# Kernel tuning notes

Hardware: AMD Instinct MI355X
Metric: run time of the kernel (lower is better)

## Reference

```python
import jax, jax.numpy as jnp
import numpy as np

H = 8          # n_heads
D_HEAD = 64    # head_dim; scores scaled by sqrt(D_HEAD)


def setup_inputs() -> dict:
    key = jax.random.key(0)
    ks = jax.random.split(key, 9)
    B, S, Dm = 8, 1024, 512
    return {
        "input_Q": jax.random.normal(ks[0], (B, S, Dm), jnp.float32),
        "input_K": jax.random.normal(ks[1], (B, S, Dm), jnp.float32),
        "input_V": jax.random.normal(ks[2], (B, S, Dm), jnp.float32),
        "attn_mask": jax.random.randint(ks[3], (B, S, S), 0, 2).astype(bool),
        "edge_encoding": jax.random.normal(ks[4], (B, S, S), jnp.float32),
        "W_Q": jax.random.normal(ks[5], (Dm, Dm), jnp.float32) / np.sqrt(Dm),
        "W_K": jax.random.normal(ks[6], (Dm, Dm), jnp.float32) / np.sqrt(Dm),
        "W_V": jax.random.normal(ks[7], (Dm, Dm), jnp.float32) / np.sqrt(Dm),
        "W_fc": jax.random.normal(ks[8], (Dm, Dm), jnp.float32) / np.sqrt(Dm),
    }


def reference(input_Q, input_K, input_V, attn_mask, edge_encoding, W_Q, W_K, W_V, W_fc):
    B, S, Dm = input_Q.shape
    # project and split heads: [B, H, S, d_head]
    def heads(x, W):
        return (x @ W).reshape(B, S, H, D_HEAD).transpose(0, 2, 1, 3)
    Q = heads(input_Q, W_Q)
    K = heads(input_K, W_K)
    V = heads(input_V, W_V)
    scores = jnp.einsum("bhqd,bhkd->bhqk", Q, K) / np.sqrt(D_HEAD)
    scores = scores + edge_encoding[:, None, :, :]
    scores = jnp.where(attn_mask[:, None, :, :], jnp.float32(-1e9), scores)
    attn = jax.nn.softmax(scores, axis=-1)
    context = jnp.einsum("bhqk,bhkd->bhqd", attn, V)
    context = context.transpose(0, 2, 1, 3).reshape(B, S, Dm)
    output = context @ W_fc
    scores_avg = scores.sum(axis=1) / H  # [B, S, S]
    return output, scores_avg
```

## Files before the change

### kernel.cpp

```cpp
#include <hip/hip_runtime.h>
#include <math.h>

#define B_ 8
#define S_ 1024
#define DM 512
#define H_ 8
#define DH 64

typedef _Float16 h4 __attribute__((ext_vector_type(4)));
typedef _Float16 h8 __attribute__((ext_vector_type(8)));
typedef float f4 __attribute__((ext_vector_type(4)));

#define MFMA16(a, b, c) __builtin_amdgcn_mfma_f32_16x16x32_f16(a, b, c, 0, 0, 0)

__global__ __launch_bounds__(256) void cast_x(
    const float* __restrict__ x0, const float* __restrict__ x1,
    const float* __restrict__ x2, _Float16* __restrict__ y0,
    _Float16* __restrict__ y1, _Float16* __restrict__ y2) {
  const float* x = (blockIdx.y == 0) ? x0 : (blockIdx.y == 1) ? x1 : x2;
  _Float16* y = (blockIdx.y == 0) ? y0 : (blockIdx.y == 1) ? y1 : y2;
  size_t i = (size_t)blockIdx.x * 1024 + (size_t)threadIdx.x * 4;
  float4 v = *(const float4*)(x + i);
  h4 hv = {(_Float16)v.x, (_Float16)v.y, (_Float16)v.z, (_Float16)v.w};
  *(h4*)(y + i) = hv;
}

__global__ __launch_bounds__(256) void cast_w(
    const float* __restrict__ w0, const float* __restrict__ w1,
    const float* __restrict__ w2, const float* __restrict__ w3,
    _Float16* __restrict__ t0, _Float16* __restrict__ t1,
    _Float16* __restrict__ t2, _Float16* __restrict__ t3) {
  const float* W;
  _Float16* T;
  switch (blockIdx.z) {
    case 0: W = w0; T = t0; break;
    case 1: W = w1; T = t1; break;
    case 2: W = w2; T = t2; break;
    default: W = w3; T = t3; break;
  }
  __shared__ _Float16 ts[64][72];
  const int t = threadIdx.x;
  const int r = t >> 2, c0 = (t & 3) * 16;
  const int n0 = blockIdx.x * 64, k0 = blockIdx.y * 64;
#pragma unroll
  for (int i = 0; i < 4; i++) {
    float4 v = *(const float4*)&W[(size_t)(k0 + r) * 512 + n0 + c0 + i * 4];
    h4 hv = {(_Float16)v.x, (_Float16)v.y, (_Float16)v.z, (_Float16)v.w};
    *(h4*)&ts[r][c0 + i * 4] = hv;
  }
  __syncthreads();
  alignas(16) _Float16 outv[16];
#pragma unroll
  for (int i = 0; i < 16; i++) outv[i] = ts[c0 + i][r];
  *(uint4*)&T[(size_t)(n0 + r) * 512 + k0 + c0] = *(uint4*)&outv[0];
  *(uint4*)&T[(size_t)(n0 + r) * 512 + k0 + c0 + 8] = *(uint4*)&outv[8];
}

__global__ __launch_bounds__(256) void gemm_qkv(
    const _Float16* __restrict__ Xq, const _Float16* __restrict__ Xk,
    const _Float16* __restrict__ Xv, const _Float16* __restrict__ Wt,
    _Float16* __restrict__ Qh, _Float16* __restrict__ Kh,
    _Float16* __restrict__ Vth) {
  const int z = blockIdx.z;
  const _Float16* A = (z == 0) ? Xq : (z == 1) ? Xk : Xv;
  const _Float16* Bt = Wt + (size_t)z * 512 * 512;
  __shared__ _Float16 As[128][72], Bs[128][72];
  const int t = threadIdx.x, lane = t & 63, w = t >> 6;
  const int quad = lane >> 4, l16 = lane & 15;
  const int row0 = blockIdx.y * 128, col0 = blockIdx.x * 128;
  const int wm = (w & 1) * 64, wn = (w >> 1) * 64;
  const int gr = t >> 3, gc = (t & 7) * 8;
  f4 acc[4][4] = {};
  uint4 pa[4], pb[4];
#pragma unroll
  for (int i = 0; i < 4; i++) {
    pa[i] = *(const uint4*)&A[(size_t)(row0 + gr + 32 * i) * DM + gc];
    pb[i] = *(const uint4*)&Bt[(size_t)(col0 + gr + 32 * i) * DM + gc];
  }
  for (int k0 = 0; k0 < DM; k0 += 64) {
    __syncthreads();
#pragma unroll
    for (int i = 0; i < 4; i++) {
      *(uint4*)&As[gr + 32 * i][gc] = pa[i];
      *(uint4*)&Bs[gr + 32 * i][gc] = pb[i];
    }
    __syncthreads();
    if (k0 + 64 < DM) {
#pragma unroll
      for (int i = 0; i < 4; i++) {
        pa[i] = *(const uint4*)&A[(size_t)(row0 + gr + 32 * i) * DM + k0 + 64 + gc];
        pb[i] = *(const uint4*)&Bt[(size_t)(col0 + gr + 32 * i) * DM + k0 + 64 + gc];
      }
    }
    h8 af[4][2], bf[4][2];
#pragma unroll
    for (int m = 0; m < 4; m++) {
      af[m][0] = *(h8*)&As[wm + m * 16 + l16][quad * 8];
      af[m][1] = *(h8*)&As[wm + m * 16 + l16][32 + quad * 8];
    }
#pragma unroll
    for (int n = 0; n < 4; n++) {
      bf[n][0] = *(h8*)&Bs[wn + n * 16 + l16][quad * 8];
      bf[n][1] = *(h8*)&Bs[wn + n * 16 + l16][32 + quad * 8];
    }
#pragma unroll
    for (int m = 0; m < 4; m++)
#pragma unroll
      for (int n = 0; n < 4; n++) {
        acc[m][n] = MFMA16(af[m][0], bf[n][0], acc[m][n]);
        acc[m][n] = MFMA16(af[m][1], bf[n][1], acc[m][n]);
      }
  }
  if (z < 2) {
    _Float16* C = (z == 0) ? Qh : Kh;
#pragma unroll
    for (int m = 0; m < 4; m++)
#pragma unroll
      for (int n = 0; n < 4; n++)
#pragma unroll
        for (int reg = 0; reg < 4; reg++) {
          size_t row = row0 + wm + m * 16 + quad * 4 + reg;
          size_t col = col0 + wn + n * 16 + l16;
          C[row * DM + col] = (_Float16)acc[m][n][reg];
        }
  } else {
#pragma unroll
    for (int m = 0; m < 4; m++)
#pragma unroll
      for (int n = 0; n < 4; n++) {
        int row = row0 + wm + m * 16 + quad * 4;
        int b = row >> 10, s = row & 1023;
        int col = col0 + wn + n * 16 + l16;
        int h = col >> 6, d = col & 63;
        h4 vv = {(_Float16)acc[m][n][0], (_Float16)acc[m][n][1],
                 (_Float16)acc[m][n][2], (_Float16)acc[m][n][3]};
        *(h4*)&Vth[((size_t)(b * 8 + h) * 64 + d) * S_ + s] = vv;
      }
  }
}

__global__ __launch_bounds__(256) void gemm_fc(
    const _Float16* __restrict__ A, const _Float16* __restrict__ Bt,
    float* __restrict__ C) {
  __shared__ _Float16 As[64][72], Bs[128][72];
  const int t = threadIdx.x, lane = t & 63, w = t >> 6;
  const int quad = lane >> 4, l16 = lane & 15;
  const int row0 = blockIdx.y * 64, col0 = blockIdx.x * 128;
  const int wm = (w & 1) * 32, wn = (w >> 1) * 64;
  const int gr = t >> 3, gc = (t & 7) * 8;
  f4 acc[2][4] = {};
  uint4 pa[2], pb[4];
#pragma unroll
  for (int i = 0; i < 2; i++)
    pa[i] = *(const uint4*)&A[(size_t)(row0 + gr + 32 * i) * DM + gc];
#pragma unroll
  for (int i = 0; i < 4; i++)
    pb[i] = *(const uint4*)&Bt[(size_t)(col0 + gr + 32 * i) * DM + gc];
  for (int k0 = 0; k0 < DM; k0 += 64) {
    __syncthreads();
#pragma unroll
    for (int i = 0; i < 2; i++) *(uint4*)&As[gr + 32 * i][gc] = pa[i];
#pragma unroll
    for (int i = 0; i < 4; i++) *(uint4*)&Bs[gr + 32 * i][gc] = pb[i];
    __syncthreads();
    if (k0 + 64 < DM) {
#pragma unroll
      for (int i = 0; i < 2; i++)
        pa[i] = *(const uint4*)&A[(size_t)(row0 + gr + 32 * i) * DM + k0 + 64 + gc];
#pragma unroll
      for (int i = 0; i < 4; i++)
        pb[i] = *(const uint4*)&Bt[(size_t)(col0 + gr + 32 * i) * DM + k0 + 64 + gc];
    }
    h8 af[2][2], bf[4][2];
#pragma unroll
    for (int m = 0; m < 2; m++) {
      af[m][0] = *(h8*)&As[wm + m * 16 + l16][quad * 8];
      af[m][1] = *(h8*)&As[wm + m * 16 + l16][32 + quad * 8];
    }
#pragma unroll
    for (int n = 0; n < 4; n++) {
      bf[n][0] = *(h8*)&Bs[wn + n * 16 + l16][quad * 8];
      bf[n][1] = *(h8*)&Bs[wn + n * 16 + l16][32 + quad * 8];
    }
#pragma unroll
    for (int m = 0; m < 2; m++)
#pragma unroll
      for (int n = 0; n < 4; n++) {
        acc[m][n] = MFMA16(af[m][0], bf[n][0], acc[m][n]);
        acc[m][n] = MFMA16(af[m][1], bf[n][1], acc[m][n]);
      }
  }
#pragma unroll
  for (int m = 0; m < 2; m++)
#pragma unroll
    for (int n = 0; n < 4; n++)
#pragma unroll
      for (int reg = 0; reg < 4; reg++) {
        size_t row = row0 + wm + m * 16 + quad * 4 + reg;
        size_t col = col0 + wn + n * 16 + l16;
        C[row * DM + col] = acc[m][n][reg];
      }
}

__global__ __launch_bounds__(256) void scores_mfma(
    const _Float16* __restrict__ Qh, const _Float16* __restrict__ Kh,
    const int* __restrict__ mask, const float* __restrict__ edge,
    float* __restrict__ out1, _Float16* __restrict__ Eh) {
  const int b = blockIdx.z;
  const int i0 = blockIdx.y * 128, j0 = blockIdx.x * 128;
  const _Float16* A = Qh + (size_t)b * S_ * DM;
  const _Float16* Bt = Kh + (size_t)b * S_ * DM;
  __shared__ _Float16 As[128][72], Bs[128][72];
  const int t = threadIdx.x, lane = t & 63, w = t >> 6;
  const int quad = lane >> 4, l16 = lane & 15;
  const int wm = (w & 1) * 64, wn = (w >> 1) * 64;
  const int gr = t >> 3, gc = (t & 7) * 8;
  f4 acc[4][4] = {};
  uint4 pa[4], pb[4];
#pragma unroll
  for (int i = 0; i < 4; i++) {
    pa[i] = *(const uint4*)&A[(size_t)(i0 + gr + 32 * i) * DM + gc];
    pb[i] = *(const uint4*)&Bt[(size_t)(j0 + gr + 32 * i) * DM + gc];
  }
  for (int k0 = 0; k0 < DM; k0 += 64) {
    __syncthreads();
#pragma unroll
    for (int i = 0; i < 4; i++) {
      *(uint4*)&As[gr + 32 * i][gc] = pa[i];
      *(uint4*)&Bs[gr + 32 * i][gc] = pb[i];
    }
    __syncthreads();
    if (k0 + 64 < DM) {
#pragma unroll
      for (int i = 0; i < 4; i++) {
        pa[i] = *(const uint4*)&A[(size_t)(i0 + gr + 32 * i) * DM + k0 + 64 + gc];
        pb[i] = *(const uint4*)&Bt[(size_t)(j0 + gr + 32 * i) * DM + k0 + 64 + gc];
      }
    }
    h8 af[4][2], bf[4][2];
#pragma unroll
    for (int m = 0; m < 4; m++) {
      af[m][0] = *(h8*)&As[wm + m * 16 + l16][quad * 8];
      af[m][1] = *(h8*)&As[wm + m * 16 + l16][32 + quad * 8];
    }
#pragma unroll
    for (int n = 0; n < 4; n++) {
      bf[n][0] = *(h8*)&Bs[wn + n * 16 + l16][quad * 8];
      bf[n][1] = *(h8*)&Bs[wn + n * 16 + l16][32 + quad * 8];
    }
#pragma unroll
    for (int m = 0; m < 4; m++)
#pragma unroll
      for (int n = 0; n < 4; n++) {
        acc[m][n] = MFMA16(af[m][0], bf[n][0], acc[m][n]);
        acc[m][n] = MFMA16(af[m][1], bf[n][1], acc[m][n]);
      }
  }
#pragma unroll
  for (int m = 0; m < 4; m++)
#pragma unroll
    for (int reg = 0; reg < 4; reg++) {
      size_t gi = i0 + wm + m * 16 + quad * 4 + reg;
      size_t rowb = ((size_t)b * S_ + gi) * S_;
#pragma unroll
      for (int n = 0; n < 4; n++) {
        size_t idx = rowb + j0 + wn + n * 16 + l16;
        int mk = mask[idx];
        float e = edge[idx];
        out1[idx] = mk ? -1e9f : (acc[m][n][reg] * (1.0f / 64.0f) + e);
        Eh[idx] = mk ? (_Float16)(-65504.0f) : (_Float16)e;
      }
    }
}

__global__ __launch_bounds__(256) void flash_mfma(
    const _Float16* __restrict__ Qh, const _Float16* __restrict__ Kh,
    const _Float16* __restrict__ Vth, const _Float16* __restrict__ Eh,
    _Float16* __restrict__ ctxh) {
  __shared__ _Float16 Ps[128][72], Ks[64][72], Vt[64][72];
  const int t = threadIdx.x, lane = t & 63, w = t >> 6;
  const int quad = lane >> 4, l16 = lane & 15;
  const int bh = blockIdx.y, b = bh >> 3, h = bh & 7;
  const int q0 = blockIdx.x * 128;
  const size_t bS = (size_t)b * S_;
  const int sr = t >> 3, sc = (t & 7) * 8;
  const int qw = w * 32;

#pragma unroll
  for (int i = 0; i < 4; i++)
    *(uint4*)&Ps[sr + 32 * i][sc] =
        *(const uint4*)&Qh[(bS + q0 + sr + 32 * i) * DM + h * DH + sc];
  __syncthreads();
  h8 aq[2][2];
#pragma unroll
  for (int m = 0; m < 2; m++)
#pragma unroll
    for (int k = 0; k < 2; k++)
      aq[m][k] = *(h8*)&Ps[qw + m * 16 + l16][k * 32 + quad * 8];

  uint4 kv[4];
  kv[0] = *(const uint4*)&Kh[(bS + sr) * DM + h * DH + sc];
  kv[1] = *(const uint4*)&Kh[(bS + sr + 32) * DM + h * DH + sc];
  kv[2] = *(const uint4*)&Vth[((size_t)bh * 64 + sr) * S_ + sc];
  kv[3] = *(const uint4*)&Vth[((size_t)bh * 64 + sr + 32) * S_ + sc];
  _Float16 evh[32];
#pragma unroll
  for (int m = 0; m < 2; m++)
#pragma unroll
    for (int n = 0; n < 4; n++)
#pragma unroll
      for (int reg = 0; reg < 4; reg++)
        evh[m * 16 + n * 4 + reg] =
            Eh[(bS + q0 + qw + m * 16 + quad * 4 + reg) * S_ + n * 16 + l16];

  f4 acco[2][4] = {};
  float m_run[2][4], l_run[2][4];
#pragma unroll
  for (int m = 0; m < 2; m++)
#pragma unroll
    for (int r = 0; r < 4; r++) {
      m_run[m][r] = -INFINITY;
      l_run[m][r] = 0.f;
    }

  for (int kb = 0; kb < S_; kb += 64) {
    __syncthreads();
    *(uint4*)&Ks[sr][sc] = kv[0];
    *(uint4*)&Ks[sr + 32][sc] = kv[1];
    *(uint4*)&Vt[sr][sc] = kv[2];
    *(uint4*)&Vt[sr + 32][sc] = kv[3];
    __syncthreads();
    const int kn = kb + 64;
    _Float16 evn[32];
    if (kn < S_) {
      kv[0] = *(const uint4*)&Kh[(bS + kn + sr) * DM + h * DH + sc];
      kv[1] = *(const uint4*)&Kh[(bS + kn + sr + 32) * DM + h * DH + sc];
      kv[2] = *(const uint4*)&Vth[((size_t)bh * 64 + sr) * S_ + kn + sc];
      kv[3] = *(const uint4*)&Vth[((size_t)bh * 64 + sr + 32) * S_ + kn + sc];
#pragma unroll
      for (int m = 0; m < 2; m++)
#pragma unroll
        for (int n = 0; n < 4; n++)
#pragma unroll
          for (int reg = 0; reg < 4; reg++)
            evn[m * 16 + n * 4 + reg] =
                Eh[(bS + q0 + qw + m * 16 + quad * 4 + reg) * S_ + kn +
                   n * 16 + l16];
    }
    f4 accs[2][4] = {};
#pragma unroll
    for (int n = 0; n < 4; n++) {
      h8 b0 = *(h8*)&Ks[n * 16 + l16][quad * 8];
      h8 b1 = *(h8*)&Ks[n * 16 + l16][32 + quad * 8];
#pragma unroll
      for (int m = 0; m < 2; m++) {
        accs[m][n] = MFMA16(aq[m][0], b0, accs[m][n]);
        accs[m][n] = MFMA16(aq[m][1], b1, accs[m][n]);
      }
    }
    float sv[2][4][4];
#pragma unroll
    for (int m = 0; m < 2; m++)
#pragma unroll
      for (int n = 0; n < 4; n++)
#pragma unroll
        for (int reg = 0; reg < 4; reg++)
          sv[m][n][reg] =
              accs[m][n][reg] * 0.125f + (float)evh[m * 16 + n * 4 + reg];
#pragma unroll
    for (int m = 0; m < 2; m++)
#pragma unroll
      for (int reg = 0; reg < 4; reg++) {
        float mx = fmaxf(fmaxf(sv[m][0][reg], sv[m][1][reg]),
                         fmaxf(sv[m][2][reg], sv[m][3][reg]));
#pragma unroll
        for (int off = 1; off < 16; off <<= 1)
          mx = fmaxf(mx, __shfl_xor(mx, off, 16));
        float mnew = fmaxf(m_run[m][reg], mx);
        float alpha = __expf(m_run[m][reg] - mnew);
        m_run[m][reg] = mnew;
        float psum = 0.f;
#pragma unroll
        for (int n = 0; n < 4; n++) {
          float p = __expf(sv[m][n][reg] - mnew);
          sv[m][n][reg] = p;
          psum += p;
        }
#pragma unroll
        for (int off = 1; off < 16; off <<= 1)
          psum += __shfl_xor(psum, off, 16);
        l_run[m][reg] = l_run[m][reg] * alpha + psum;
#pragma unroll
        for (int d = 0; d < 4; d++) acco[m][d][reg] *= alpha;
      }
#pragma unroll
    for (int m = 0; m < 2; m++)
#pragma unroll
      for (int n = 0; n < 4; n++)
#pragma unroll
        for (int reg = 0; reg < 4; reg++)
          Ps[qw + m * 16 + quad * 4 + reg][n * 16 + l16] =
              (_Float16)sv[m][n][reg];
    h8 ap[2][2];
#pragma unroll
    for (int m = 0; m < 2; m++)
#pragma unroll
      for (int k = 0; k < 2; k++)
        ap[m][k] = *(h8*)&Ps[qw + m * 16 + l16][k * 32 + quad * 8];
#pragma unroll
    for (int d = 0; d < 4; d++) {
      h8 bv0 = *(h8*)&Vt[d * 16 + l16][quad * 8];
      h8 bv1 = *(h8*)&Vt[d * 16 + l16][32 + quad * 8];
#pragma unroll
      for (int m = 0; m < 2; m++) {
        acco[m][d] = MFMA16(ap[m][0], bv0, acco[m][d]);
        acco[m][d] = MFMA16(ap[m][1], bv1, acco[m][d]);
      }
    }
    if (kn < S_) {
#pragma unroll
      for (int i = 0; i < 32; i++) evh[i] = evn[i];
    }
  }
#pragma unroll
  for (int m = 0; m < 2; m++)
#pragma unroll
    for (int d = 0; d < 4; d++)
#pragma unroll
      for (int reg = 0; reg < 4; reg++) {
        float o = acco[m][d][reg] / l_run[m][reg];
        ctxh[(bS + q0 + qw + m * 16 + quad * 4 + reg) * DM + h * DH + d * 16 +
             l16] = (_Float16)o;
      }
}

extern "C" void kernel_launch(void* const* d_in, const int* in_sizes, int n_in,
                              void* d_out, int out_size, void* d_ws,
                              size_t ws_size, hipStream_t stream) {
  const float* Xq = (const float*)d_in[0];
  const float* Xk = (const float*)d_in[1];
  const float* Xv = (const float*)d_in[2];
  const int* mask = (const int*)d_in[3];
  const float* edge = (const float*)d_in[4];
  const float* Wq = (const float*)d_in[5];
  const float* Wk = (const float*)d_in[6];
  const float* Wv = (const float*)d_in[7];
  const float* Wfc = (const float*)d_in[8];

  float* out0 = (float*)d_out;
  float* out1 = out0 + (size_t)B_ * S_ * DM;

  const size_t NE = (size_t)B_ * S_ * DM;
  char* ws = (char*)d_ws;
  _Float16* Qh = (_Float16*)ws;
  _Float16* Kh = Qh + NE;
  _Float16* Vth = Kh + NE;
  _Float16* Xhq = Vth + NE;
  _Float16* Xhk = Xhq + NE;
  _Float16* Xhv = Xhk + NE;
  _Float16* Wt = Xhv + NE;
  _Float16* Wtf = Wt + 3 * 512 * 512;
  _Float16* Eh = Wt + 4 * 512 * 512;
  _Float16* ctxh = Xhq;

  dim3 blk(256);
  cast_x<<<dim3(4096, 3), blk, 0, stream>>>(Xq, Xk, Xv, Xhq, Xhk, Xhv);
  cast_w<<<dim3(8, 8, 4), blk, 0, stream>>>(Wq, Wk, Wv, Wfc, Wt,
                                            Wt + 512 * 512, Wt + 2 * 512 * 512,
                                            Wtf);
  gemm_qkv<<<dim3(4, 64, 3), blk, 0, stream>>>(Xhq, Xhk, Xhv, Wt, Qh, Kh, Vth);
  scores_mfma<<<dim3(8, 8, 8), blk, 0, stream>>>(Qh, Kh, mask, edge, out1, Eh);
  flash_mfma<<<dim3(8, 64), blk, 0, stream>>>(Qh, Kh, Vth, Eh, ctxh);
  gemm_fc<<<dim3(4, 128), blk, 0, stream>>>(ctxh, Wtf, out0);
}
```

Baseline: 402.6 us.

## Tile edge-bias buffer per key block and remap block order for L2 locality

The fp16 edge/mask bias buffer is now written by the scores kernel in a tiled layout: per batch, per 64-key tile, per query row, with each lane's four columns stored contiguously. The flash kernel can then load them as h4 vectors instead of 32 scattered scalar fp16 loads per step. Block-index swizzles are also added to gemm_qkv, gemm_fc, scores and flash so that blocks scheduled together share operand tiles (heads of the same batch, neighbouring rows) in L2. The scores kernel's scattered fp16 writes become less coalesced, which is a possible cost.

Result: faster. 389.9 us (-3.2%).

```diff
diff --git a/kernel.cpp b/kernel.cpp
--- a/kernel.cpp
+++ b/kernel.cpp
@@ -62,12 +62,16 @@
     _Float16* __restrict__ Qh, _Float16* __restrict__ Kh,
     _Float16* __restrict__ Vth) {
   const int z = blockIdx.z;
+  const int id = blockIdx.x + 4 * blockIdx.y;
+  const int c = id & 7, r = id >> 3;
+  const int by = c + 8 * (r & 7);
+  const int bx = r >> 3;
   const _Float16* A = (z == 0) ? Xq : (z == 1) ? Xk : Xv;
   const _Float16* Bt = Wt + (size_t)z * 512 * 512;
   __shared__ _Float16 As[128][72], Bs[128][72];
   const int t = threadIdx.x, lane = t & 63, w = t >> 6;
   const int quad = lane >> 4, l16 = lane & 15;
-  const int row0 = blockIdx.y * 128, col0 = blockIdx.x * 128;
+  const int row0 = by * 128, col0 = bx * 128;
   const int wm = (w & 1) * 64, wn = (w >> 1) * 64;
   const int gr = t >> 3, gc = (t & 7) * 8;
   f4 acc[4][4] = {};
@@ -142,10 +146,14 @@
 __global__ __launch_bounds__(256) void gemm_fc(
     const _Float16* __restrict__ A, const _Float16* __restrict__ Bt,
     float* __restrict__ C) {
+  const int id = blockIdx.x + 4 * blockIdx.y;
+  const int c = id & 7, r = id >> 3;
+  const int by = c + 8 * (r & 15);
+  const int bx = r >> 4;
   __shared__ _Float16 As[64][72], Bs[128][72];
   const int t = threadIdx.x, lane = t & 63, w = t >> 6;
   const int quad = lane >> 4, l16 = lane & 15;
-  const int row0 = blockIdx.y * 64, col0 = blockIdx.x * 128;
+  const int row0 = by * 64, col0 = bx * 128;
   const int wm = (w & 1) * 32, wn = (w >> 1) * 64;
   const int gr = t >> 3, gc = (t & 7) * 8;
   f4 acc[2][4] = {};
@@ -205,9 +213,11 @@
 __global__ __launch_bounds__(256) void scores_mfma(
     const _Float16* __restrict__ Qh, const _Float16* __restrict__ Kh,
     const int* __restrict__ mask, const float* __restrict__ edge,
-    float* __restrict__ out1, _Float16* __restrict__ Eh) {
+    float* __restrict__ out1, _Float16* __restrict__ Ehs) {
   const int b = blockIdx.z;
-  const int i0 = blockIdx.y * 128, j0 = blockIdx.x * 128;
+  const int id = blockIdx.x + 8 * blockIdx.y;
+  const int iy = id & 7, jx = id >> 3;
+  const int i0 = iy * 128, j0 = jx * 128;
   const _Float16* A = Qh + (size_t)b * S_ * DM;
   const _Float16* Bt = Kh + (size_t)b * S_ * DM;
   __shared__ _Float16 As[128][72], Bs[128][72];
@@ -256,32 +266,39 @@
         acc[m][n] = MFMA16(af[m][1], bf[n][1], acc[m][n]);
       }
   }
+  const int jt_base = j0 >> 6;
 #pragma unroll
   for (int m = 0; m < 4; m++)
 #pragma unroll
     for (int reg = 0; reg < 4; reg++) {
       size_t gi = i0 + wm + m * 16 + quad * 4 + reg;
       size_t rowb = ((size_t)b * S_ + gi) * S_;
+      const int jt = jt_base + (wn >> 6);
+      size_t ehrow = (((size_t)b * 16 + jt) * 1024 + gi) * 64 + l16 * 4;
 #pragma unroll
       for (int n = 0; n < 4; n++) {
         size_t idx = rowb + j0 + wn + n * 16 + l16;
         int mk = mask[idx];
         float e = edge[idx];
         out1[idx] = mk ? -1e9f : (acc[m][n][reg] * (1.0f / 64.0f) + e);
-        Eh[idx] = mk ? (_Float16)(-65504.0f) : (_Float16)e;
+        Ehs[ehrow + n] = mk ? (_Float16)(-65504.0f) : (_Float16)e;
       }
     }
 }
 
 __global__ __launch_bounds__(256) void flash_mfma(
     const _Float16* __restrict__ Qh, const _Float16* __restrict__ Kh,
-    const _Float16* __restrict__ Vth, const _Float16* __restrict__ Eh,
+    const _Float16* __restrict__ Vth, const _Float16* __restrict__ Ehs,
     _Float16* __restrict__ ctxh) {
   __shared__ _Float16 Ps[128][72], Ks[64][72], Vt[64][72];
   const int t = threadIdx.x, lane = t & 63, w = t >> 6;
   const int quad = lane >> 4, l16 = lane & 15;
-  const int bh = blockIdx.y, b = bh >> 3, h = bh & 7;
-  const int q0 = blockIdx.x * 128;
+  const int g = blockIdx.x + 8 * blockIdx.y;
+  const int c = g & 7, r = g >> 3;
+  const int bh = c + 8 * (r & 7);
+  const int qb = r >> 3;
+  const int b = bh >> 3, h = bh & 7;
+  const int q0 = qb * 128;
   const size_t bS = (size_t)b * S_;
   const int sr = t >> 3, sc = (t & 7) * 8;
   const int qw = w * 32;
@@ -303,24 +320,24 @@
   kv[1] = *(const uint4*)&Kh[(bS + sr + 32) * DM + h * DH + sc];
   kv[2] = *(const uint4*)&Vth[((size_t)bh * 64 + sr) * S_ + sc];
   kv[3] = *(const uint4*)&Vth[((size_t)bh * 64 + sr + 32) * S_ + sc];
-  _Float16 evh[32];
+  h4 evh[2][4];
 #pragma unroll
   for (int m = 0; m < 2; m++)
 #pragma unroll
-    for (int n = 0; n < 4; n++)
-#pragma unroll
-      for (int reg = 0; reg < 4; reg++)
-        evh[m * 16 + n * 4 + reg] =
-            Eh[(bS + q0 + qw + m * 16 + quad * 4 + reg) * S_ + n * 16 + l16];
+    for (int reg = 0; reg < 4; reg++)
+      evh[m][reg] = *(const h4*)&Ehs[(((size_t)b * 16 + 0) * 1024 + q0 + qw +
+                                      m * 16 + quad * 4 + reg) *
+                                         64 +
+                                     l16 * 4];
 
   f4 acco[2][4] = {};
   float m_run[2][4], l_run[2][4];
 #pragma unroll
   for (int m = 0; m < 2; m++)
 #pragma unroll
-    for (int r = 0; r < 4; r++) {
-      m_run[m][r] = -INFINITY;
-      l_run[m][r] = 0.f;
+    for (int rr = 0; rr < 4; rr++) {
+      m_run[m][rr] = -INFINITY;
+      l_run[m][rr] = 0.f;
     }
 
   for (int kb = 0; kb < S_; kb += 64) {
@@ -331,21 +348,20 @@
     *(uint4*)&Vt[sr + 32][sc] = kv[3];
     __syncthreads();
     const int kn = kb + 64;
-    _Float16 evn[32];
+    h4 evn[2][4];
     if (kn < S_) {
       kv[0] = *(const uint4*)&Kh[(bS + kn + sr) * DM + h * DH + sc];
       kv[1] = *(const uint4*)&Kh[(bS + kn + sr + 32) * DM + h * DH + sc];
       kv[2] = *(const uint4*)&Vth[((size_t)bh * 64 + sr) * S_ + kn + sc];
       kv[3] = *(const uint4*)&Vth[((size_t)bh * 64 + sr + 32) * S_ + kn + sc];
+      const size_t ehb = ((size_t)b * 16 + (kn >> 6)) * 1024;
 #pragma unroll
       for (int m = 0; m < 2; m++)
 #pragma unroll
-        for (int n = 0; n < 4; n++)
-#pragma unroll
-          for (int reg = 0; reg < 4; reg++)
-            evn[m * 16 + n * 4 + reg] =
-                Eh[(bS + q0 + qw + m * 16 + quad * 4 + reg) * S_ + kn +
-                   n * 16 + l16];
+        for (int reg = 0; reg < 4; reg++)
+          evn[m][reg] =
+              *(const h4*)&Ehs[(ehb + q0 + qw + m * 16 + quad * 4 + reg) * 64 +
+                               l16 * 4];
     }
     f4 accs[2][4] = {};
 #pragma unroll
@@ -365,8 +381,7 @@
       for (int n = 0; n < 4; n++)
 #pragma unroll
         for (int reg = 0; reg < 4; reg++)
-          sv[m][n][reg] =
-              accs[m][n][reg] * 0.125f + (float)evh[m * 16 + n * 4 + reg];
+          sv[m][n][reg] = accs[m][n][reg] * 0.125f + (float)evh[m][reg][n];
 #pragma unroll
     for (int m = 0; m < 2; m++)
 #pragma unroll
@@ -419,7 +434,9 @@
     }
     if (kn < S_) {
 #pragma unroll
-      for (int i = 0; i < 32; i++) evh[i] = evn[i];
+      for (int m = 0; m < 2; m++)
+#pragma unroll
+        for (int reg = 0; reg < 4; reg++) evh[m][reg] = evn[m][reg];
     }
   }
 #pragma unroll
@@ -460,7 +477,7 @@
   _Float16* Xhv = Xhk + NE;
   _Float16* Wt = Xhv + NE;
   _Float16* Wtf = Wt + 3 * 512 * 512;
-  _Float16* Eh = Wt + 4 * 512 * 512;
+  _Float16* Ehs = Wt + 4 * 512 * 512;
   _Float16* ctxh = Xhq;
 
   dim3 blk(256);
@@ -469,7 +486,8 @@
                                             Wt + 512 * 512, Wt + 2 * 512 * 512,
                                             Wtf);
   gemm_qkv<<<dim3(4, 64, 3), blk, 0, stream>>>(Xhq, Xhk, Xhv, Wt, Qh, Kh, Vth);
-  scores_mfma<<<dim3(8, 8, 8), blk, 0, stream>>>(Qh, Kh, mask, edge, out1, Eh);
-  flash_mfma<<<dim3(8, 64), blk, 0, stream>>>(Qh, Kh, Vth, Eh, ctxh);
+  scores_mfma<<<dim3(8, 8, 8), blk, 0, stream>>>(Qh, Kh, mask, edge, out1,
+                                                 Ehs);
+  flash_mfma<<<dim3(8, 64), blk, 0, stream>>>(Qh, Kh, Vth, Ehs, ctxh);
   gemm_fc<<<dim3(4, 128), blk, 0, stream>>>(ctxh, Wtf, out0);
 }
```
